# Performance work log

Hardware: AMD Instinct MI355X
Metric: run time of the kernel (lower is better)

The kernel has to match this reference:

```python
import jax, jax.numpy as jnp
import numpy as np

NUM_HEADS = 16
LN_EPS = 1e-5


def _layer_norm(x, g, b):
    m = x.mean(-1, keepdims=True)
    v = x.var(-1, keepdims=True)
    return (x - m) / jnp.sqrt(v + LN_EPS) * g + b


def setup_inputs() -> dict:
    key = jax.random.key(0)
    ks = jax.random.split(key, 4)
    Bq, Bk, Nk, C = 128, 128, 256, 1024
    return {
        "qx": jax.random.normal(ks[0], (Bq, 1, C), jnp.float32),
        "kx": jax.random.normal(ks[1], (Bk, Nk, C), jnp.float32),
        "gq": jnp.ones((C,), jnp.float32),
        "bq": jnp.zeros((C,), jnp.float32),
        "gk": jnp.ones((C,), jnp.float32),
        "bk": jnp.zeros((C,), jnp.float32),
        "Wq": jax.random.normal(ks[2], (C, C), jnp.float32) * (C ** -0.5),
        "Wk": jax.random.normal(ks[3], (C, C), jnp.float32) * (C ** -0.5),
    }


def reference(qx, kx, gq, bq, gk, bk, Wq, Wk):
    H = NUM_HEADS
    Bq, _, C = qx.shape  # qx: [Bq, 1, C]
    Bk, Nk, _ = kx.shape  # kx: [Bk, Nk, C]
    hd = C // H
    scale = hd ** -0.5
    # LayerNorm + linear projections (nn.Linear: x @ W.T, no bias)
    q = (_layer_norm(qx, gq, bq) @ Wq.T).reshape(Bq, H, hd)       # [Bq, H, hd] (Nq=1 squeezed)
    k = (_layer_norm(kx, gk, bk) @ Wk.T).reshape(Bk, Nk, H, hd)   # [Bk, Nk, H, hd]
    # Full bipartite cross-batch attention scores: [Bq, Bk, H, Nk]
    attn = jnp.einsum('qhc,knhc->qkhn', q, k) * scale
    attn = jax.nn.softmax(attn, axis=-1)
    # v = kx broadcast over heads in original einsum 'khnc,qkhn->qkc';
    # equivalent: sum attn over heads, then contract over Nk.
    w = attn.sum(axis=2)                                           # [Bq, Bk, Nk]
    x = jnp.einsum('knc,qkn->qkc', kx, w)                          # [Bq, Bk, C]
    return x
```

## Files before the change

kernel.cpp:

```cpp
#include <hip/hip_runtime.h>


typedef unsigned short ushort_t;
typedef __bf16 bf16x8 __attribute__((ext_vector_type(8)));
typedef float f32x4 __attribute__((ext_vector_type(4)));

#define AS1 __attribute__((address_space(1)))
#define AS3 __attribute__((address_space(3)))

__device__ __forceinline__ void gload_lds16(const void* g, void* l) {
  __builtin_amdgcn_global_load_lds((const AS1 unsigned int*)g, (AS3 unsigned int*)l, 16, 0, 0);
}

__device__ __forceinline__ ushort_t f2bf(float f) {
  unsigned u = __float_as_uint(f);
  unsigned r = u + 0x7FFFu + ((u >> 16) & 1u);
  return (ushort_t)(r >> 16);
}

__global__ __launch_bounds__(256) void cvt_bf16_kernel(const float* __restrict__ src,
                                                       ushort_t* __restrict__ dst, int n4) {
  int i = blockIdx.x * 256 + threadIdx.x;
  if (i < n4) {
    float4 v = ((const float4*)src)[i];
    ushort4 o;
    o.x = f2bf(v.x); o.y = f2bf(v.y); o.z = f2bf(v.z); o.w = f2bf(v.w);
    ((ushort4*)dst)[i] = o;
  }
}

__global__ __launch_bounds__(256) void ln_kernel(const float* __restrict__ kx,
                                                 const float* __restrict__ qx,
                                                 const float* __restrict__ gk,
                                                 const float* __restrict__ bk,
                                                 const float* __restrict__ gq,
                                                 const float* __restrict__ bq,
                                                 ushort_t* __restrict__ kln,
                                                 ushort_t* __restrict__ qln) {
  int row = blockIdx.x;
  const float* src; ushort_t* dst; const float* g; const float* bb;
  if (row < 32768) {
    src = kx + (size_t)row * 1024; dst = kln + (size_t)row * 1024; g = gk; bb = bk;
  } else {
    int r = row - 32768;
    src = qx + (size_t)r * 1024; dst = qln + (size_t)r * 1024; g = gq; bb = bq;
  }
  int tid = threadIdx.x;
  float4 v = ((const float4*)src)[tid];
  float s  = v.x + v.y + v.z + v.w;
  float s2 = v.x*v.x + v.y*v.y + v.z*v.z + v.w*v.w;
  #pragma unroll
  for (int off = 1; off < 64; off <<= 1) {
    s  += __shfl_xor(s, off);
    s2 += __shfl_xor(s2, off);
  }
  __shared__ float red[8];
  int wid = tid >> 6, lane = tid & 63;
  if (lane == 0) { red[wid] = s; red[4 + wid] = s2; }
  __syncthreads();
  s  = red[0] + red[1] + red[2] + red[3];
  s2 = red[4] + red[5] + red[6] + red[7];
  float mean = s * (1.0f / 1024.0f);
  float var  = s2 * (1.0f / 1024.0f) - mean * mean;
  float rstd = rsqrtf(var + 1e-5f);
  float4 gg = ((const float4*)g)[tid];
  float4 b4 = ((const float4*)bb)[tid];
  ushort4 o;
  o.x = f2bf((v.x - mean) * rstd * gg.x + b4.x);
  o.y = f2bf((v.y - mean) * rstd * gg.y + b4.y);
  o.z = f2bf((v.z - mean) * rstd * gg.z + b4.z);
  o.w = f2bf((v.w - mean) * rstd * gg.w + b4.w);
  ((ushort4*)dst)[tid] = o;
}

#define BM 128
#define BN 128
#define BK 32

__global__ __launch_bounds__(256) void gemm_bt_kernel(const ushort_t* __restrict__ A,
                                                      const ushort_t* __restrict__ Bt,
                                                      ushort_t* __restrict__ C,
                                                      int M, int N, int K) {
  __shared__ ushort_t As[2][BM * BK];
  __shared__ ushort_t Bs[2][BN * BK];
  const int tid  = threadIdx.x;
  const int lane = tid & 63;
  const int wid  = tid >> 6;

  const int Mt = M >> 7, Nt = N >> 7;
  const int nwg = Mt * Nt;
  const int qq = nwg >> 3, r8 = nwg & 7;
  const int xcd = blockIdx.x & 7, idx = blockIdx.x >> 3;
  const int wg = (xcd < r8 ? xcd * (qq + 1) : r8 * (qq + 1) + (xcd - r8) * qq) + idx;
  const int mt = wg / Nt, nt = wg - mt * Nt;
  const size_t m0 = (size_t)mt * BM, n0 = (size_t)nt * BN;

  const int NTILE = K / BK;
  const int rlo = lane >> 2;
  const int cl  = lane & 3;

  f32x4 acc[4][4];
  #pragma unroll
  for (int i = 0; i < 4; ++i)
    #pragma unroll
    for (int j = 0; j < 4; ++j) acc[i][j] = (f32x4){0.f, 0.f, 0.f, 0.f};

  #pragma unroll
  for (int c = 0; c < 2; ++c) {
    int row = (wid << 5) + (c << 4) + rlo;
    int gch = cl ^ (row & 3);
    gload_lds16(A  + (m0 + row) * (size_t)K + gch * 8, &As[0][((wid << 5) + (c << 4)) * BK]);
    gload_lds16(Bt + (n0 + row) * (size_t)K + gch * 8, &Bs[0][((wid << 5) + (c << 4)) * BK]);
  }

  const int g = lane >> 4, rr = lane & 15;
  const int wr = wid >> 1, wc = wid & 1;

  for (int t = 0; t < NTILE; ++t) {
    __syncthreads();
    if (t + 1 < NTILE) {
      int k0 = (t + 1) * BK;
      #pragma unroll
      for (int c = 0; c < 2; ++c) {
        int row = (wid << 5) + (c << 4) + rlo;
        int gch = cl ^ (row & 3);
        gload_lds16(A  + (m0 + row) * (size_t)K + k0 + gch * 8,
                    &As[(t + 1) & 1][((wid << 5) + (c << 4)) * BK]);
        gload_lds16(Bt + (n0 + row) * (size_t)K + k0 + gch * 8,
                    &Bs[(t + 1) & 1][((wid << 5) + (c << 4)) * BK]);
      }
    }
    const ushort_t* as = As[t & 1];
    const ushort_t* bs = Bs[t & 1];
    bf16x8 af[4], bfr[4];
    #pragma unroll
    for (int i = 0; i < 4; ++i) {
      int rowA = (wr << 6) + (i << 4) + rr;
      int chA  = g ^ (rowA & 3);
      af[i] = *(const bf16x8*)&as[rowA * BK + chA * 8];
      int rowB = (wc << 6) + (i << 4) + rr;
      int chB  = g ^ (rowB & 3);
      bfr[i] = *(const bf16x8*)&bs[rowB * BK + chB * 8];
    }
    #pragma unroll
    for (int i = 0; i < 4; ++i)
      #pragma unroll
      for (int j = 0; j < 4; ++j)
        acc[i][j] = __builtin_amdgcn_mfma_f32_16x16x32_bf16(af[i], bfr[j], acc[i][j], 0, 0, 0);
  }

  #pragma unroll
  for (int i = 0; i < 4; ++i)
    #pragma unroll
    for (int j = 0; j < 4; ++j)
      #pragma unroll
      for (int rg = 0; rg < 4; ++rg) {
        size_t row = m0 + (wr << 6) + (i << 4) + (g << 2) + rg;
        size_t col = n0 + (wc << 6) + (j << 4) + rr;
        C[row * (size_t)N + col] = f2bf(acc[i][j][rg]);
      }
}

__global__ __launch_bounds__(256, 3) void scores_kernel(const ushort_t* __restrict__ qp,
                                                        const ushort_t* __restrict__ kk,
                                                        ushort_t* __restrict__ wbuf) {
  __shared__ float pbuf[2][16][258];

  const int tid = threadIdx.x, lane = tid & 63, wid = tid >> 6;
  const int g = lane >> 4, rr = lane & 15;

  const int b = blockIdx.x;
  const int wg = (b & 7) * 128 + (b >> 3);
  const int kb = wg >> 3;
  const int q0 = (wg & 7) << 4;

  const int hs = wid;

  float w_acc[16][4];
  #pragma unroll
  for (int t = 0; t < 16; ++t)
    #pragma unroll
    for (int r = 0; r < 4; ++r) w_acc[t][r] = 0.f;

  const ushort_t* qrow = qp + (size_t)(q0 + rr) * 1024;
  const ushort_t* krow = kk + ((size_t)kb * 256 + rr) * 1024;

  for (int hp = 0; hp < 4; ++hp) {
    const int h = hp * 4 + hs;
    const int co = h * 64 + g * 8;
    bf16x8 aq0 = *(const bf16x8*)(qrow + co);
    bf16x8 aq1 = *(const bf16x8*)(qrow + co + 32);
    f32x4 s[16];
    #pragma unroll
    for (int t = 0; t < 16; ++t) {
      const ushort_t* kr = krow + (size_t)(t * 16) * 1024 + co;
      bf16x8 b0 = *(const bf16x8*)(kr);
      bf16x8 b1 = *(const bf16x8*)(kr + 32);
      f32x4 a = (f32x4){0.f, 0.f, 0.f, 0.f};
      a = __builtin_amdgcn_mfma_f32_16x16x32_bf16(aq0, b0, a, 0, 0, 0);
      a = __builtin_amdgcn_mfma_f32_16x16x32_bf16(aq1, b1, a, 0, 0, 0);
      s[t] = a;
    }
    #pragma unroll
    for (int r = 0; r < 4; ++r) {
      float mx = s[0][r];
      #pragma unroll
      for (int t = 1; t < 16; ++t) mx = fmaxf(mx, s[t][r]);
      mx = fmaxf(mx, __shfl_xor(mx, 1));
      mx = fmaxf(mx, __shfl_xor(mx, 2));
      mx = fmaxf(mx, __shfl_xor(mx, 4));
      mx = fmaxf(mx, __shfl_xor(mx, 8));
      float sum = 0.f;
      float e[16];
      #pragma unroll
      for (int t = 0; t < 16; ++t) {
        e[t] = __expf((s[t][r] - mx) * 0.125f);
        sum += e[t];
      }
      sum += __shfl_xor(sum, 1);
      sum += __shfl_xor(sum, 2);
      sum += __shfl_xor(sum, 4);
      sum += __shfl_xor(sum, 8);
      float inv = 1.0f / sum;
      #pragma unroll
      for (int t = 0; t < 16; ++t) w_acc[t][r] += e[t] * inv;
    }
  }

  __syncthreads();
  if (hs >= 2) {
    #pragma unroll
    for (int t = 0; t < 16; ++t)
      #pragma unroll
      for (int r = 0; r < 4; ++r)
        pbuf[hs - 2][(g << 2) + r][t * 16 + rr] = w_acc[t][r];
  }
  __syncthreads();
  if (hs < 2) {
    #pragma unroll
    for (int t = 0; t < 16; ++t)
      #pragma unroll
      for (int r = 0; r < 4; ++r)
        w_acc[t][r] += pbuf[hs][(g << 2) + r][t * 16 + rr];
    if (hs == 1) {
      #pragma unroll
      for (int t = 0; t < 16; ++t)
        #pragma unroll
        for (int r = 0; r < 4; ++r)
          pbuf[1][(g << 2) + r][t * 16 + rr] = w_acc[t][r];
    }
  }
  __syncthreads();
  if (hs == 0) {
    ushort_t* wb = wbuf + (size_t)kb * 32768;
    #pragma unroll
    for (int t = 0; t < 16; ++t)
      #pragma unroll
      for (int r = 0; r < 4; ++r) {
        float v = w_acc[t][r] + pbuf[1][(g << 2) + r][t * 16 + rr];
        wb[(size_t)(q0 + (g << 2) + r) * 256 + t * 16 + rr] = f2bf(v);
      }
  }
}

__global__ __launch_bounds__(256, 4) void pv_kernel(const ushort_t* __restrict__ wbuf,
                                                    const float* __restrict__ kx,
                                                    float* __restrict__ xout) {
  const int tid = threadIdx.x, lane = tid & 63, wid = tid >> 6;
  const int g = lane >> 4, rr = lane & 15;

  const int b = blockIdx.x;
  const int wg = (b & 7) * 128 + (b >> 3);
  const int kb = wg >> 3;
  const int c0 = (wg & 7) * 128;

  const int wr = wid >> 1, wc = wid & 1;

  f32x4 acc[4][4];
  #pragma unroll
  for (int i = 0; i < 4; ++i)
    #pragma unroll
    for (int j = 0; j < 4; ++j) acc[i][j] = (f32x4){0.f, 0.f, 0.f, 0.f};

  const ushort_t* wb = wbuf + (size_t)kb * 32768;
  const float* kxb = kx + (size_t)kb * 256 * 1024;

  for (int nc = 0; nc < 8; ++nc) {
    const int n0 = nc * 32 + g * 8;
    bf16x8 af[4];
    #pragma unroll
    for (int i = 0; i < 4; ++i) {
      int q = (wr << 6) + (i << 4) + rr;
      af[i] = *(const bf16x8*)(wb + (size_t)q * 256 + n0);
    }
    #pragma unroll
    for (int j = 0; j < 4; ++j) {
      int c = c0 + (wc << 6) + (j << 4) + rr;
      const float* src = kxb + (size_t)n0 * 1024 + c;
      float f[8];
      #pragma unroll
      for (int jj = 0; jj < 8; ++jj) f[jj] = src[(size_t)jj * 1024];
      bf16x8 bb;
      #pragma unroll
      for (int jj = 0; jj < 8; ++jj) bb[jj] = (__bf16)f[jj];
      #pragma unroll
      for (int i = 0; i < 4; ++i)
        acc[i][j] = __builtin_amdgcn_mfma_f32_16x16x32_bf16(af[i], bb, acc[i][j], 0, 0, 0);
    }
  }

  #pragma unroll
  for (int i = 0; i < 4; ++i)
    #pragma unroll
    for (int j = 0; j < 4; ++j)
      #pragma unroll
      for (int rg = 0; rg < 4; ++rg) {
        int q = (wr << 6) + (i << 4) + (g << 2) + rg;
        int c = c0 + (wc << 6) + (j << 4) + rr;
        xout[((size_t)q * 128 + kb) * 1024 + c] = acc[i][j][rg];
      }
}

extern "C" void kernel_launch(void* const* d_in, const int* in_sizes, int n_in,
                              void* d_out, int out_size, void* d_ws, size_t ws_size,
                              hipStream_t stream) {
  const float* qx = (const float*)d_in[0];
  const float* kx = (const float*)d_in[1];
  const float* gq = (const float*)d_in[2];
  const float* bq = (const float*)d_in[3];
  const float* gk = (const float*)d_in[4];
  const float* bk = (const float*)d_in[5];
  const float* Wq = (const float*)d_in[6];
  const float* Wk = (const float*)d_in[7];

  char* ws = (char*)d_ws;
  ushort_t* kkp   = (ushort_t*)(ws);
  ushort_t* qproj = (ushort_t*)(ws + 67108864);
  ushort_t* wbuf  = (ushort_t*)(ws + 67371008);
  ushort_t* qln   = (ushort_t*)(ws + 67371008);
  ushort_t* Wqb   = (ushort_t*)(ws + 67371008 + 262144);
  ushort_t* Wkb   = (ushort_t*)(ws + 67371008 + 2359296);
  ushort_t* kln  = (ushort_t*)d_out;
  float*    xout = (float*)d_out;

  cvt_bf16_kernel<<<1024, 256, 0, stream>>>(Wq, Wqb, 262144);
  cvt_bf16_kernel<<<1024, 256, 0, stream>>>(Wk, Wkb, 262144);
  ln_kernel<<<32896, 256, 0, stream>>>(kx, qx, gk, bk, gq, bq, kln, qln);
  gemm_bt_kernel<<<8, 256, 0, stream>>>(qln, Wqb, qproj, 128, 1024, 1024);
  gemm_bt_kernel<<<2048, 256, 0, stream>>>(kln, Wkb, kkp, 32768, 1024, 1024);
  scores_kernel<<<1024, 256, 0, stream>>>(qproj, kkp, wbuf);
  pv_kernel<<<1024, 256, 0, stream>>>(wbuf, kx, xout);
}
```

Baseline: 301.9 us.

## Use 256x256-tile 512-thread pipelined GEMM for the large K projection

Adds a new bf16 GEMM kernel with 256x256 output tiles, 8 waves, and a 4-stage LDS ring filled by direct global-to-LDS loads, and uses it for the 32768x1024x1024 key projection. Each block now covers four times the output area of the old 128x128 tiles, which raises operand reuse and cuts global traffic. Loads for future k-steps are interleaved with the MFMA halves, with priority raising and explicit vmcnt waits. The cost is 128 accumulator vectors per thread, so register pressure and occupancy may suffer, and there are only 512 workgroups.

```diff
diff --git a/kernel.cpp b/kernel.cpp
--- a/kernel.cpp
+++ b/kernel.cpp
@@ -161,6 +161,142 @@
       }
 }
 
+__global__ __launch_bounds__(512, 2) void gemm256_kernel(const ushort_t* __restrict__ A,
+                                                         const ushort_t* __restrict__ Bt,
+                                                         ushort_t* __restrict__ C,
+                                                         int M, int N) {
+  __shared__ ushort_t lds[4][2][256 * 32];
+
+  const int tid = threadIdx.x, lane = tid & 63, wid = tid >> 6;
+  const int g = lane >> 4, rr = lane & 15;
+  const int wr = wid >> 2, wc = wid & 3;
+
+  const int Mt = M >> 8, Nt = N >> 8;
+  const int nwg = Mt * Nt;
+  const int qq = nwg >> 3, r8 = nwg & 7;
+  const int xcd = blockIdx.x & 7, idx = blockIdx.x >> 3;
+  const int wg = (xcd < r8 ? xcd * (qq + 1) : r8 * (qq + 1) + (xcd - r8) * qq) + idx;
+  const int mt = wg / Nt, nt = wg - mt * Nt;
+  const size_t m0 = (size_t)mt << 8, n0 = (size_t)nt << 8;
+
+  const int s_r  = lane >> 2;
+  const int s_gr = (lane & 3) ^ (s_r & 3);
+
+  const ushort_t* Abase = A  + m0 * 1024;
+  const ushort_t* Bbase = Bt + n0 * 1024;
+
+  f32x4 acc[8][4];
+  #pragma unroll
+  for (int i = 0; i < 8; ++i)
+    #pragma unroll
+    for (int j = 0; j < 4; ++j) acc[i][j] = (f32x4){0.f, 0.f, 0.f, 0.f};
+
+  auto stageA = [&](int kt) {
+    const int k0 = kt << 5;
+    ushort_t* dst = &lds[kt & 3][0][0];
+    #pragma unroll
+    for (int it = 0; it < 2; ++it) {
+      int ci = (wid << 1) | it;
+      int r  = (ci << 4) + s_r;
+      gload_lds16(Abase + (size_t)r * 1024 + k0 + (s_gr << 3), dst + (ci << 9));
+    }
+  };
+  auto stageB = [&](int kt) {
+    const int k0 = kt << 5;
+    ushort_t* dst = &lds[kt & 3][1][0];
+    #pragma unroll
+    for (int it = 0; it < 2; ++it) {
+      int ci = (wid << 1) | it;
+      int r  = (ci << 4) + s_r;
+      gload_lds16(Bbase + (size_t)r * 1024 + k0 + (s_gr << 3), dst + (ci << 9));
+    }
+  };
+
+  stageA(0); stageB(0); stageA(1); stageB(1); stageA(2); stageB(2);
+  asm volatile("s_waitcnt vmcnt(8)" ::: "memory");
+  __builtin_amdgcn_s_barrier();
+
+  const int rsw = (rr & 3);
+
+  #pragma unroll 1
+  for (int u = 0; u < 29; ++u) {
+    const ushort_t* as = &lds[u & 3][0][0];
+    const ushort_t* bs = &lds[u & 3][1][0];
+    bf16x8 af[8];
+    {
+      #pragma unroll
+      for (int i = 0; i < 8; ++i) {
+        int r = (wr << 7) + (i << 4) + rr;
+        af[i] = *(const bf16x8*)&as[(r << 5) + ((g ^ rsw) << 3)];
+      }
+      int r0 = (wc << 6) + rr;
+      bf16x8 b0 = *(const bf16x8*)&bs[(r0 << 5) + ((g ^ rsw) << 3)];
+      int r1 = (wc << 6) + 16 + rr;
+      bf16x8 b1 = *(const bf16x8*)&bs[(r1 << 5) + ((g ^ rsw) << 3)];
+      stageA(u + 3);
+      __builtin_amdgcn_s_setprio(1);
+      #pragma unroll
+      for (int i = 0; i < 8; ++i) {
+        acc[i][0] = __builtin_amdgcn_mfma_f32_16x16x32_bf16(af[i], b0, acc[i][0], 0, 0, 0);
+        acc[i][1] = __builtin_amdgcn_mfma_f32_16x16x32_bf16(af[i], b1, acc[i][1], 0, 0, 0);
+      }
+      __builtin_amdgcn_s_setprio(0);
+      __builtin_amdgcn_s_barrier();
+    }
+    {
+      int r2 = (wc << 6) + 32 + rr;
+      bf16x8 b2 = *(const bf16x8*)&bs[(r2 << 5) + ((g ^ rsw) << 3)];
+      int r3 = (wc << 6) + 48 + rr;
+      bf16x8 b3 = *(const bf16x8*)&bs[(r3 << 5) + ((g ^ rsw) << 3)];
+      stageB(u + 3);
+      __builtin_amdgcn_s_setprio(1);
+      #pragma unroll
+      for (int i = 0; i < 8; ++i) {
+        acc[i][2] = __builtin_amdgcn_mfma_f32_16x16x32_bf16(af[i], b2, acc[i][2], 0, 0, 0);
+        acc[i][3] = __builtin_amdgcn_mfma_f32_16x16x32_bf16(af[i], b3, acc[i][3], 0, 0, 0);
+      }
+      __builtin_amdgcn_s_setprio(0);
+      asm volatile("s_waitcnt vmcnt(8)" ::: "memory");
+      __builtin_amdgcn_s_barrier();
+    }
+  }
+
+  asm volatile("s_waitcnt vmcnt(0)" ::: "memory");
+  __builtin_amdgcn_s_barrier();
+  #pragma unroll 1
+  for (int u = 29; u < 32; ++u) {
+    const ushort_t* as = &lds[u & 3][0][0];
+    const ushort_t* bs = &lds[u & 3][1][0];
+    bf16x8 af2[8], bfj[4];
+    #pragma unroll
+    for (int i = 0; i < 8; ++i) {
+      int r = (wr << 7) + (i << 4) + rr;
+      af2[i] = *(const bf16x8*)&as[(r << 5) + ((g ^ rsw) << 3)];
+    }
+    #pragma unroll
+    for (int j = 0; j < 4; ++j) {
+      int r = (wc << 6) + (j << 4) + rr;
+      bfj[j] = *(const bf16x8*)&bs[(r << 5) + ((g ^ rsw) << 3)];
+    }
+    #pragma unroll
+    for (int i = 0; i < 8; ++i)
+      #pragma unroll
+      for (int j = 0; j < 4; ++j)
+        acc[i][j] = __builtin_amdgcn_mfma_f32_16x16x32_bf16(af2[i], bfj[j], acc[i][j], 0, 0, 0);
+  }
+
+  #pragma unroll
+  for (int i = 0; i < 8; ++i)
+    #pragma unroll
+    for (int j = 0; j < 4; ++j)
+      #pragma unroll
+      for (int rg = 0; rg < 4; ++rg) {
+        size_t row = m0 + (wr << 7) + (i << 4) + (g << 2) + rg;
+        size_t col = n0 + (wc << 6) + (j << 4) + rr;
+        C[row * (size_t)N + col] = f2bf(acc[i][j][rg]);
+      }
+}
+
 __global__ __launch_bounds__(256, 3) void scores_kernel(const ushort_t* __restrict__ qp,
                                                         const ushort_t* __restrict__ kk,
                                                         ushort_t* __restrict__ wbuf) {
@@ -347,7 +483,7 @@
   cvt_bf16_kernel<<<1024, 256, 0, stream>>>(Wk, Wkb, 262144);
   ln_kernel<<<32896, 256, 0, stream>>>(kx, qx, gk, bk, gq, bq, kln, qln);
   gemm_bt_kernel<<<8, 256, 0, stream>>>(qln, Wqb, qproj, 128, 1024, 1024);
-  gemm_bt_kernel<<<2048, 256, 0, stream>>>(kln, Wkb, kkp, 32768, 1024, 1024);
+  gemm256_kernel<<<512, 512, 0, stream>>>(kln, Wkb, kkp, 32768, 1024);
   scores_kernel<<<1024, 256, 0, stream>>>(qproj, kkp, wbuf);
   pv_kernel<<<1024, 256, 0, stream>>>(wbuf, kx, xout);
 }
```

Result: faster. 290.3 us (-3.9%).
